# Optimization experiments

Measured on AMD Instinct MI355X. Metric: run time of the kernel, lower is better.

Reference implementation:

```python
import jax, jax.numpy as jnp
import numpy as np

B, S, D, H = 4, 2048, 1024, 16
HD = D // H  # 64

def setup_inputs() -> dict:
    key = jax.random.key(0)
    ks = jax.random.split(key, 6)
    scale = 1.0 / np.sqrt(D)
    return {
        "x": jax.random.normal(ks[0], (B, S, D), dtype=jnp.float32),
        "Wq": jax.random.normal(ks[1], (D, D), dtype=jnp.float32) * scale,
        "Wk": jax.random.normal(ks[2], (D, D), dtype=jnp.float32) * scale,
        "Wv": jax.random.normal(ks[3], (D, D), dtype=jnp.float32) * scale,
        "Wo": jax.random.normal(ks[4], (D, D), dtype=jnp.float32) * scale,
        "bo": jnp.zeros((D,), dtype=jnp.float32),
    }

def reference(x, Wq, Wk, Wv, Wo, bo):
    b, s, d = x.shape
    # projections (no bias for q/k/v, matching QKV_BIAS=False)
    q = (x @ Wq).reshape(b, s, H, HD).transpose(0, 2, 1, 3)  # [b,h,s,hd]
    k = (x @ Wk).reshape(b, s, H, HD).transpose(0, 2, 1, 3)
    v = (x @ Wv).reshape(b, s, H, HD).transpose(0, 2, 1, 3)
    scores = jnp.einsum('bhqd,bhkd->bhqk', q, k)  # [b,h,s,s]
    causal = jnp.tril(jnp.ones((s, s), dtype=bool))  # True where allowed
    scores = jnp.where(causal, scores, -jnp.inf)
    attn = jax.nn.softmax(scores / np.sqrt(HD), axis=-1)
    ctx = jnp.einsum('bhqk,bhkd->bhqd', attn, v)  # [b,h,s,hd]
    ctx = ctx.transpose(0, 2, 1, 3).reshape(b, s, d)
    return ctx @ Wo + bo
```

## Files before the change

kernel.cpp:

```cpp
#include <hip/hip_runtime.h>

#define BSZ 4
#define SEQ 2048
#define DIM 1024
#define NH  16
#define HD  64
#define QT  128
#define KT  64
#define PAD 72
#define NKT (DIM / 64)

typedef float v4f __attribute__((ext_vector_type(4)));
typedef short s8v __attribute__((ext_vector_type(8)));
typedef unsigned short u16;
typedef unsigned short u16x8 __attribute__((ext_vector_type(8)));
typedef unsigned short u16x4 __attribute__((ext_vector_type(4)));
typedef unsigned int u32;

__device__ __forceinline__ u16 f2bf(float f) {
  u32 u = __builtin_bit_cast(u32, f);
  u32 r = u + 0x7fffu + ((u >> 16) & 1u);
  return (u16)(r >> 16);
}
__device__ __forceinline__ float bf2f(u16 h) {
  return __builtin_bit_cast(float, (u32)h << 16);
}
__device__ __forceinline__ float fast_exp2(float x) {
#if __has_builtin(__builtin_amdgcn_exp2f)
  return __builtin_amdgcn_exp2f(x);
#else
  return exp2f(x);
#endif
}
__device__ __forceinline__ void gll16(const u16* g, u16* l) {
  __builtin_amdgcn_global_load_lds((const __attribute__((address_space(1))) void*)g,
                                   (__attribute__((address_space(3))) void*)l, 16, 0, 0);
}
__device__ __forceinline__ void wg_barrier() { asm volatile("s_barrier" ::: "memory"); }
#define WAITCNT_VM4   0xF74
#define WAITCNT_VM0   0xF70
#define WAITCNT_LGKM0 0xC07F

__global__ __launch_bounds__(256) void cast_bf16_kernel(const float* __restrict__ x,
                                                        u16* __restrict__ o, int n4) {
  int i = blockIdx.x * 256 + threadIdx.x;
  if (i >= n4) return;
  v4f v = reinterpret_cast<const v4f*>(x)[i];
  u16x4 r;
  #pragma unroll
  for (int c = 0; c < 4; c++) r[c] = f2bf(v[c]);
  reinterpret_cast<u16x4*>(o)[i] = r;
}

__global__ __launch_bounds__(256) void transpose_cast_kernel(const float* __restrict__ W0,
                                                             const float* __restrict__ W1,
                                                             const float* __restrict__ W2,
                                                             const float* __restrict__ W3,
                                                             u16* __restrict__ out) {
  const float* W = blockIdx.z == 0 ? W0 : blockIdx.z == 1 ? W1 : blockIdx.z == 2 ? W2 : W3;
  const float scale = (blockIdx.z == 0) ? 0.18033688011112042f : 1.0f;
  u16* T = out + (size_t)blockIdx.z * DIM * DIM;
  __shared__ float tile[32][33];
  int tx = threadIdx.x & 31, ty = threadIdx.x >> 5;
  int bn = blockIdx.x * 32, bk = blockIdx.y * 32;
  #pragma unroll
  for (int r = 0; r < 4; r++) {
    int k = bk + ty + r * 8;
    tile[ty + r * 8][tx] = W[(size_t)k * DIM + bn + tx];
  }
  __syncthreads();
  #pragma unroll
  for (int r = 0; r < 4; r++) {
    int n = bn + ty + r * 8;
    T[(size_t)n * DIM + bk + tx] = f2bf(tile[tx][ty + r * 8] * scale);
  }
}


#define ST_A(t_, kc_)                                                             \
  gll16(Ag0 + (t_) * 64 + (kc_) * 32, Aw0 + ((t_)&1) * 16384 + (kc_) * 8192);     \
  gll16(Ag1 + (t_) * 64 + (kc_) * 32, Aw1 + ((t_)&1) * 16384 + (kc_) * 8192);
#define ST_B(t_, kc_)                                                             \
  gll16(Bg0 + (t_) * 64 + (kc_) * 32, Bw0 + ((t_)&1) * 16384 + (kc_) * 8192);     \
  gll16(Bg1 + (t_) * 64 + (kc_) * 32, Bw1 + ((t_)&1) * 16384 + (kc_) * 8192);

#define PH(t_, kc_, mh_, STAGES, TAILW)                                           \
  { const u16* Ab = AL + ((t_)&1) * 16384 + (kc_) * 8192 + aRd;                   \
    const u16* Bb = BL + ((t_)&1) * 16384 + (kc_) * 8192 + bRd;                   \
    s8v af[4], bf[4];                                                             \
    _Pragma("unroll") for (int i_ = 0; i_ < 4; i_++)                              \
      af[i_] = *(const s8v*)(Ab + ((mh_) * 4 + i_) * 512);                        \
    _Pragma("unroll") for (int j_ = 0; j_ < 4; j_++)                              \
      bf[j_] = *(const s8v*)(Bb + j_ * 512);                                      \
    STAGES                                                                        \
    wg_barrier();                                                                 \
    __builtin_amdgcn_s_waitcnt(WAITCNT_LGKM0);                                    \
    __builtin_amdgcn_s_setprio(1);                                                \
    _Pragma("unroll") for (int i_ = 0; i_ < 4; i_++)                              \
      _Pragma("unroll") for (int j_ = 0; j_ < 4; j_++)                            \
        acc[(mh_) * 4 + i_][j_] = __builtin_amdgcn_mfma_f32_16x16x32_bf16(        \
            af[i_], bf[j_], acc[(mh_) * 4 + i_][j_], 0, 0, 0);                    \
    __builtin_amdgcn_s_setprio(0);                                                \
    TAILW                                                                         \
    wg_barrier(); }

#define GEMM256_CORE()                                                            \
  extern __shared__ __align__(16) u16 lds[];                                      \
  const int t = threadIdx.x;                                                      \
  const int lane = t & 63, w = t >> 6;                                            \
  const int waveM = w >> 2, waveN = w & 3;                                        \
  const int quad = lane >> 4, l16 = lane & 15;                                    \
  const int sR = lane & 15, sC = lane >> 4;                                       \
  u16* AL = lds;                                                                  \
  u16* BL = lds + 32768;                                                          \
  v4f acc[8][4];                                                                  \
  _Pragma("unroll") for (int i = 0; i < 8; i++)                                   \
    _Pragma("unroll") for (int j = 0; j < 4; j++)                                 \
      acc[i][j] = (v4f){0.f, 0.f, 0.f, 0.f};                                      \
  const u16* Ag0 = A + (size_t)(m0 + w * 32 + sR) * DIM + sC * 8;                 \
  const u16* Ag1 = A + (size_t)(m0 + w * 32 + 16 + sR) * DIM + sC * 8;            \
  const u16* Bg0 = Bt + (size_t)(n0 + w * 32 + sR) * DIM + sC * 8;                \
  const u16* Bg1 = Bt + (size_t)(n0 + w * 32 + 16 + sR) * DIM + sC * 8;           \
  u16* Aw0 = AL + (w * 2 + 0) * 512;                                              \
  u16* Aw1 = AL + (w * 2 + 1) * 512;                                              \
  u16* Bw0 = BL + (w * 2 + 0) * 512;                                              \
  u16* Bw1 = BL + (w * 2 + 1) * 512;                                              \
  const int aRd = waveM * 4096 + quad * 128 + l16 * 8;                            \
  const int bRd = waveN * 2048 + quad * 128 + l16 * 8;                            \
  ST_A(0, 0) ST_B(0, 0) ST_A(0, 1) ST_B(0, 1) ST_A(1, 0) ST_B(1, 0)              \
  __builtin_amdgcn_s_waitcnt(WAITCNT_VM4);                                        \
  wg_barrier();                                                                   \
  _Pragma("unroll 2") for (int kt = 0; kt < NKT - 2; kt++) {                      \
    PH(kt, 0, 0, ST_A(kt + 1, 1), )                                               \
    PH(kt, 0, 1, ST_B(kt + 1, 1), )                                               \
    PH(kt, 1, 0, ST_A(kt + 2, 0), )                                               \
    PH(kt, 1, 1, ST_B(kt + 2, 0), __builtin_amdgcn_s_waitcnt(WAITCNT_VM4);)       \
  }                                                                               \
  PH(NKT - 2, 0, 0, ST_A(NKT - 1, 1), )                                           \
  PH(NKT - 2, 0, 1, ST_B(NKT - 1, 1), )                                           \
  PH(NKT - 2, 1, 0, , )                                                           \
  PH(NKT - 2, 1, 1, , __builtin_amdgcn_s_waitcnt(WAITCNT_VM0);)                   \
  PH(NKT - 1, 0, 0, , )                                                           \
  PH(NKT - 1, 0, 1, , )                                                           \
  PH(NKT - 1, 1, 0, , )                                                           \
  PH(NKT - 1, 1, 1, , )

__global__ __launch_bounds__(512, 2) void gemm_qkv(const u16* __restrict__ A, const u16* __restrict__ Wt,
                                                   u16* __restrict__ Qb, u16* __restrict__ Kb,
                                                   u16* __restrict__ Vtg) {
  const int bid = blockIdx.x;
  const int swz = (bid & 7) * 48 + (bid >> 3);
  const int z = swz >> 7;
  const int rem = swz & 127;
  const int m0 = (rem >> 2) * 256;
  const int n0 = (rem & 3) * 256;
  const u16* Bt = Wt + (size_t)z * DIM * DIM;
  GEMM256_CORE()
  if (z == 2) {
    #pragma unroll
    for (int mi = 0; mi < 8; mi++) {
      #pragma unroll
      for (int ni = 0; ni < 4; ni++) {
        int gm0 = m0 + waveM * 128 + mi * 16 + quad * 4;
        int gn = n0 + waveN * 64 + ni * 16 + l16;
        int b = gm0 >> 11, s0 = gm0 & (SEQ - 1), hh = gn >> 6, d = gn & (HD - 1);
        u16x4 o;
        #pragma unroll
        for (int r = 0; r < 4; r++) o[r] = f2bf(acc[mi][ni][r]);
        *(u16x4*)(Vtg + ((size_t)(b * NH + hh) * HD + d) * SEQ + s0) = o;
      }
    }
  } else {
    u16* C = (z == 0) ? Qb : Kb;
    #pragma unroll
    for (int mi = 0; mi < 8; mi++) {
      #pragma unroll
      for (int ni = 0; ni < 4; ni++) {
        int gn = n0 + waveN * 64 + ni * 16 + l16;
        #pragma unroll
        for (int r = 0; r < 4; r++) {
          int gm = m0 + waveM * 128 + mi * 16 + quad * 4 + r;
          C[(size_t)gm * DIM + gn] = f2bf(acc[mi][ni][r]);
        }
      }
    }
  }
}

__global__ __launch_bounds__(512, 2) void gemm_proj(const u16* __restrict__ A, const u16* __restrict__ Bt,
                                                    float* __restrict__ Cf, const float* __restrict__ bias) {
  const int bid = blockIdx.x;
  const int swz = (bid & 7) * 16 + (bid >> 3);
  const int m0 = (swz >> 2) * 256;
  const int n0 = (swz & 3) * 256;
  GEMM256_CORE()
  #pragma unroll
  for (int ni = 0; ni < 4; ni++) {
    int gn = n0 + waveN * 64 + ni * 16 + l16;
    float bv = bias[gn];
    #pragma unroll
    for (int mi = 0; mi < 8; mi++) {
      #pragma unroll
      for (int r = 0; r < 4; r++) {
        int gm = m0 + waveM * 128 + mi * 16 + quad * 4 + r;
        Cf[(size_t)gm * DIM + gn] = acc[mi][ni][r] + bv;
      }
    }
  }
}

__global__ __launch_bounds__(256, 3) void flash_attn_mfma(const u16* __restrict__ Qb,
                                                          const u16* __restrict__ Kb,
                                                          const u16* __restrict__ Vtg,
                                                          u16* __restrict__ Ob) {
  const int h = blockIdx.x, px = blockIdx.y, bb = blockIdx.z;
  const int t = threadIdx.x;
  const int lane = t & 63, w = t >> 6;
  const int quad = lane >> 4, l16 = lane & 15;

  __shared__ u16 QPs[QT * PAD];
  __shared__ u16 Ks[KT * PAD];
  __shared__ u16 Vs[HD * PAD];

  const size_t qkbase = (size_t)bb * SEQ * DIM + h * HD;
  const size_t vbase = ((size_t)bb * NH + h) * (size_t)HD * SEQ;

  const int vrow = t >> 2, scol = (t & 3) * 16;
  const int krow = ((vrow >> 5) + 2 * ((vrow >> 2) & 1)) * 16 + ((vrow >> 3) & 3) * 4 + (vrow & 3);

  for (int pass = 0; pass < 2; pass++) {
    const int qi = (pass == 0) ? px : (SEQ / QT - 1 - px);
    const int q0 = qi * QT;
    const int wq = q0 + w * 32;
    const int ntiles = 2 * qi + 2;

    __syncthreads();

    {
      const int r = t >> 1, c0 = (t & 1) * 32;
      const u16* src = Qb + qkbase + (size_t)(q0 + r) * DIM + c0;
      #pragma unroll
      for (int ch = 0; ch < 4; ch++)
        *(u16x8*)(QPs + r * PAD + c0 + ch * 8) = *(const u16x8*)(src + ch * 8);
    }
    __syncthreads();

    s8v qf[2][2];
    #pragma unroll
    for (int ni = 0; ni < 2; ni++)
      #pragma unroll
      for (int kc = 0; kc < 2; kc++)
        qf[ni][kc] = *(const s8v*)(QPs + (w * 32 + ni * 16 + l16) * PAD + kc * 32 + quad * 8);

    u16x8 kr0, kr1, vr0, vr1;
    {
      const u16* kp = Kb + qkbase + (size_t)vrow * DIM + scol;
      kr0 = *(const u16x8*)kp; kr1 = *(const u16x8*)(kp + 8);
      const u16* vp = Vtg + vbase + (size_t)vrow * SEQ + scol;
      vr0 = *(const u16x8*)vp; vr1 = *(const u16x8*)(vp + 8);
    }

    float mrun[2] = {-1e30f, -1e30f}, lrun[2] = {0.f, 0.f};
    v4f O[4][2];
    #pragma unroll
    for (int di = 0; di < 4; di++)
      #pragma unroll
      for (int ni = 0; ni < 2; ni++) O[di][ni] = (v4f){0.f, 0.f, 0.f, 0.f};

    for (int it = 0; it < ntiles; ++it) {
      const int kv0 = it * KT;
      __syncthreads();
      *(u16x8*)(Ks + krow * PAD + scol) = kr0;
      *(u16x8*)(Ks + krow * PAD + scol + 8) = kr1;
      *(u16x8*)(Vs + vrow * PAD + scol) = vr0;
      *(u16x8*)(Vs + vrow * PAD + scol + 8) = vr1;
      __syncthreads();
      if (it + 1 < ntiles) {
        const int nkv = kv0 + KT;
        const u16* kp = Kb + qkbase + (size_t)(nkv + vrow) * DIM + scol;
        kr0 = *(const u16x8*)kp; kr1 = *(const u16x8*)(kp + 8);
        const u16* vp = Vtg + vbase + (size_t)vrow * SEQ + nkv + scol;
        vr0 = *(const u16x8*)vp; vr1 = *(const u16x8*)(vp + 8);
      }
      if (kv0 > wq + 31) continue;

      v4f sc[4][2];
      #pragma unroll
      for (int mi = 0; mi < 4; mi++)
        #pragma unroll
        for (int ni = 0; ni < 2; ni++) sc[mi][ni] = (v4f){0.f, 0.f, 0.f, 0.f};
      #pragma unroll
      for (int kc = 0; kc < 2; kc++) {
        #pragma unroll
        for (int mi = 0; mi < 4; mi++) {
          s8v kf = *(const s8v*)(Ks + (mi * 16 + l16) * PAD + kc * 32 + quad * 8);
          sc[mi][0] = __builtin_amdgcn_mfma_f32_16x16x32_bf16(kf, qf[0][kc], sc[mi][0], 0, 0, 0);
          sc[mi][1] = __builtin_amdgcn_mfma_f32_16x16x32_bf16(kf, qf[1][kc], sc[mi][1], 0, 0, 0);
        }
      }

      if (kv0 + KT > wq) {
        #pragma unroll
        for (int mi = 0; mi < 4; mi++) {
          const int kvb = kv0 + (mi & 1) * 32 + quad * 8 + (mi >> 1) * 4;
          #pragma unroll
          for (int ni = 0; ni < 2; ni++) {
            const int qg = wq + ni * 16 + l16;
            #pragma unroll
            for (int r = 0; r < 4; r++)
              if (kvb + r > qg) sc[mi][ni][r] = -1e30f;
          }
        }
      }

      float alpha[2];
      #pragma unroll
      for (int ni = 0; ni < 2; ni++) {
        float mx = -1e30f;
        #pragma unroll
        for (int mi = 0; mi < 4; mi++)
          #pragma unroll
          for (int r = 0; r < 4; r++) mx = fmaxf(mx, sc[mi][ni][r]);
        mx = fmaxf(mx, __shfl_xor(mx, 16, 64));
        mx = fmaxf(mx, __shfl_xor(mx, 32, 64));
        const float mnew = fmaxf(mrun[ni], mx);
        alpha[ni] = fast_exp2(mrun[ni] - mnew);
        mrun[ni] = mnew;
        float rsum = 0.f;
        #pragma unroll
        for (int mi = 0; mi < 4; mi++)
          #pragma unroll
          for (int r = 0; r < 4; r++) {
            float p = fast_exp2(sc[mi][ni][r] - mnew);
            sc[mi][ni][r] = p;
            rsum += p;
          }
        rsum += __shfl_xor(rsum, 16, 64);
        rsum += __shfl_xor(rsum, 32, 64);
        lrun[ni] = lrun[ni] * alpha[ni] + rsum;
      }
      #pragma unroll
      for (int di = 0; di < 4; di++)
        #pragma unroll
        for (int ni = 0; ni < 2; ni++)
          #pragma unroll
          for (int r = 0; r < 4; r++) O[di][ni][r] *= alpha[ni];

      s8v pf[2][2];
      #pragma unroll
      for (int ni = 0; ni < 2; ni++)
        #pragma unroll
        for (int kc = 0; kc < 2; kc++)
          #pragma unroll
          for (int j = 0; j < 8; j++)
            pf[ni][kc][j] = (short)f2bf(sc[kc + 2 * (j >> 2)][ni][j & 3]);

      #pragma unroll
      for (int kc = 0; kc < 2; kc++) {
        #pragma unroll
        for (int di = 0; di < 4; di++) {
          s8v vf = *(const s8v*)(Vs + (di * 16 + l16) * PAD + kc * 32 + quad * 8);
          O[di][0] = __builtin_amdgcn_mfma_f32_16x16x32_bf16(vf, pf[0][kc], O[di][0], 0, 0, 0);
          O[di][1] = __builtin_amdgcn_mfma_f32_16x16x32_bf16(vf, pf[1][kc], O[di][1], 0, 0, 0);
        }
      }
    }

    const float inv0 = 1.f / lrun[0], inv1 = 1.f / lrun[1];
    #pragma unroll
    for (int di = 0; di < 4; di++)
      #pragma unroll
      for (int ni = 0; ni < 2; ni++) {
        const float inv = ni ? inv1 : inv0;
        #pragma unroll
        for (int r = 0; r < 4; r++)
          QPs[(w * 32 + ni * 16 + l16) * PAD + di * 16 + quad * 4 + r] = f2bf(O[di][ni][r] * inv);
      }
    __syncthreads();
    {
      const int r = t >> 1, c0 = (t & 1) * 32;
      u16* dst = Ob + qkbase + (size_t)(q0 + r) * DIM + c0;
      #pragma unroll
      for (int ch = 0; ch < 4; ch++)
        *(u16x8*)(dst + ch * 8) = *(const u16x8*)(QPs + r * PAD + c0 + ch * 8);
    }
  }
}

extern "C" void kernel_launch(void* const* d_in, const int* in_sizes, int n_in,
                              void* d_out, int out_size, void* d_ws, size_t ws_size,
                              hipStream_t stream) {
  (void)in_sizes; (void)n_in; (void)out_size; (void)ws_size;
  const float* x  = (const float*)d_in[0];
  const float* Wq = (const float*)d_in[1];
  const float* Wk = (const float*)d_in[2];
  const float* Wv = (const float*)d_in[3];
  const float* Wo = (const float*)d_in[4];
  const float* bo = (const float*)d_in[5];
  float* out = (float*)d_out;

  static bool lds_attr_done = false;
  if (!lds_attr_done) {
    hipFuncSetAttribute(reinterpret_cast<const void*>(gemm_qkv),
                        hipFuncAttributeMaxDynamicSharedMemorySize, 131072);
    hipFuncSetAttribute(reinterpret_cast<const void*>(gemm_proj),
                        hipFuncAttributeMaxDynamicSharedMemorySize, 131072);
    lds_attr_done = true;
  }

  char* ws = (char*)d_ws;
  const size_t MB = 1024ull * 1024ull;
  u16* Xb  = (u16*)(ws);
  u16* Wt  = (u16*)(ws + 16 * MB);
  u16* Qb  = (u16*)(ws + 24 * MB);
  u16* Kb  = (u16*)(ws + 40 * MB);
  u16* Vtg = (u16*)(ws + 56 * MB);
  u16* Cb  = (u16*)(ws + 72 * MB);

  const int NTOK = BSZ * SEQ;
  const int n4 = NTOK * DIM / 4;
  cast_bf16_kernel<<<(n4 + 255) / 256, 256, 0, stream>>>(x, Xb, n4);
  transpose_cast_kernel<<<dim3(32, 32, 4), 256, 0, stream>>>(Wq, Wk, Wv, Wo, Wt);

  gemm_qkv<<<dim3(384), 512, 131072, stream>>>(Xb, Wt, Qb, Kb, Vtg);

  flash_attn_mfma<<<dim3(NH, SEQ / QT / 2, BSZ), 256, 0, stream>>>(Qb, Kb, Vtg, Cb);

  gemm_proj<<<dim3(128), 512, 131072, stream>>>(Cb, Wt + 3ull * DIM * DIM, out, bo);
}
```

Baseline: 284.4 us.

## Retile GEMMs to 256x128 with 3-stage pipeline, lazy softmax rescale, packed bf16 cvt

The QKV and output-projection GEMMs move from 256x256 tiles with a double buffer to 256x128 tiles with a triple-buffered LDS pipeline. This doubles the number of workgroups, which improves CU fill for the small projection GEMM, and changes the wait counts. The flash-attention softmax now skips rescaling O and l when the new row max exceeds the running max by no more than 8 (log2 units), which saves multiplies but risks larger intermediate values. Float-to-bf16 conversion now uses the hardware v_cvt_pk_bf16_f32 instruction instead of integer rounding code. LDS use rises to 144KB per block, and it is unclear whether two blocks still fit per CU.

Result: faster. 266.2 us (-6.4%).

```diff
diff --git a/kernel.cpp b/kernel.cpp
--- a/kernel.cpp
+++ b/kernel.cpp
@@ -16,15 +16,18 @@
 typedef unsigned short u16x8 __attribute__((ext_vector_type(8)));
 typedef unsigned short u16x4 __attribute__((ext_vector_type(4)));
 typedef unsigned int u32;
+typedef unsigned int u32x2 __attribute__((ext_vector_type(2)));
+typedef unsigned int u32x4 __attribute__((ext_vector_type(4)));
 
 __device__ __forceinline__ u16 f2bf(float f) {
   u32 u = __builtin_bit_cast(u32, f);
   u32 r = u + 0x7fffu + ((u >> 16) & 1u);
   return (u16)(r >> 16);
 }
-__device__ __forceinline__ float bf2f(u16 h) {
-  return __builtin_bit_cast(float, (u32)h << 16);
-}
+__device__ __forceinline__ u32 cvtpk(float lo, float hi) {
+  u32 r; asm("v_cvt_pk_bf16_f32 %0, %1, %2" : "=v"(r) : "v"(lo), "v"(hi)); return r;
+}
+__device__ __forceinline__ u16 f2bf1(float f) { return (u16)cvtpk(f, f); }
 __device__ __forceinline__ float fast_exp2(float x) {
 #if __has_builtin(__builtin_amdgcn_exp2f)
   return __builtin_amdgcn_exp2f(x);
@@ -37,9 +40,9 @@
                                    (__attribute__((address_space(3))) void*)l, 16, 0, 0);
 }
 __device__ __forceinline__ void wg_barrier() { asm volatile("s_barrier" ::: "memory"); }
-#define WAITCNT_VM4   0xF74
-#define WAITCNT_VM0   0xF70
 #define WAITCNT_LGKM0 0xC07F
+#define VMW6 __builtin_amdgcn_s_waitcnt(0xF76);
+#define VMW0 __builtin_amdgcn_s_waitcnt(0xF70);
 
 __global__ __launch_bounds__(256) void cast_bf16_kernel(const float* __restrict__ x,
                                                         u16* __restrict__ o, int n4) {
@@ -77,110 +80,108 @@
 }
 
 
-#define ST_A(t_, kc_)                                                             \
-  gll16(Ag0 + (t_) * 64 + (kc_) * 32, Aw0 + ((t_)&1) * 16384 + (kc_) * 8192);     \
-  gll16(Ag1 + (t_) * 64 + (kc_) * 32, Aw1 + ((t_)&1) * 16384 + (kc_) * 8192);
-#define ST_B(t_, kc_)                                                             \
-  gll16(Bg0 + (t_) * 64 + (kc_) * 32, Bw0 + ((t_)&1) * 16384 + (kc_) * 8192);     \
-  gll16(Bg1 + (t_) * 64 + (kc_) * 32, Bw1 + ((t_)&1) * 16384 + (kc_) * 8192);
-
-#define PH(t_, kc_, mh_, STAGES, TAILW)                                           \
-  { const u16* Ab = AL + ((t_)&1) * 16384 + (kc_) * 8192 + aRd;                   \
-    const u16* Bb = BL + ((t_)&1) * 16384 + (kc_) * 8192 + bRd;                   \
-    s8v af[4], bf[4];                                                             \
-    _Pragma("unroll") for (int i_ = 0; i_ < 4; i_++)                              \
-      af[i_] = *(const s8v*)(Ab + ((mh_) * 4 + i_) * 512);                        \
-    _Pragma("unroll") for (int j_ = 0; j_ < 4; j_++)                              \
-      bf[j_] = *(const s8v*)(Bb + j_ * 512);                                      \
+#define ST_TILE(t_, s_)                                                           \
+  gll16(Ag0 + (t_) * 64,      AW0 + (s_) * 16384);                                \
+  gll16(Ag1 + (t_) * 64,      AW1 + (s_) * 16384);                                \
+  gll16(Ag0 + (t_) * 64 + 32, AW0 + (s_) * 16384 + 8192);                         \
+  gll16(Ag1 + (t_) * 64 + 32, AW1 + (s_) * 16384 + 8192);                         \
+  gll16(Bg0 + (t_) * 64,      BW0 + (s_) * 8192);                                 \
+  gll16(Bg0 + (t_) * 64 + 32, BW0 + (s_) * 8192 + 4096);
+
+#define PH(t_, s_, STAGES, VMW)                                                   \
+  { const u16* Ab = AL + (s_) * 16384 + aRd;                                      \
+    const u16* Bb = BL + (s_) * 8192 + bRd;                                       \
+    s8v af[2][4], bf[2][4];                                                       \
+    _Pragma("unroll") for (int kc_ = 0; kc_ < 2; kc_++) {                         \
+      _Pragma("unroll") for (int i_ = 0; i_ < 4; i_++)                            \
+        af[kc_][i_] = *(const s8v*)(Ab + kc_ * 8192 + i_ * 512);                  \
+      _Pragma("unroll") for (int j_ = 0; j_ < 4; j_++)                            \
+        bf[kc_][j_] = *(const s8v*)(Bb + kc_ * 4096 + j_ * 512);                  \
+    }                                                                             \
     STAGES                                                                        \
+    VMW                                                                           \
     wg_barrier();                                                                 \
     __builtin_amdgcn_s_waitcnt(WAITCNT_LGKM0);                                    \
     __builtin_amdgcn_s_setprio(1);                                                \
-    _Pragma("unroll") for (int i_ = 0; i_ < 4; i_++)                              \
-      _Pragma("unroll") for (int j_ = 0; j_ < 4; j_++)                            \
-        acc[(mh_) * 4 + i_][j_] = __builtin_amdgcn_mfma_f32_16x16x32_bf16(        \
-            af[i_], bf[j_], acc[(mh_) * 4 + i_][j_], 0, 0, 0);                    \
+    _Pragma("unroll") for (int kc_ = 0; kc_ < 2; kc_++)                           \
+      _Pragma("unroll") for (int i_ = 0; i_ < 4; i_++)                            \
+        _Pragma("unroll") for (int j_ = 0; j_ < 4; j_++)                          \
+          acc[i_][j_] = __builtin_amdgcn_mfma_f32_16x16x32_bf16(                  \
+              af[kc_][i_], bf[kc_][j_], acc[i_][j_], 0, 0, 0);                    \
     __builtin_amdgcn_s_setprio(0);                                                \
-    TAILW                                                                         \
     wg_barrier(); }
 
-#define GEMM256_CORE()                                                            \
+#define GEMM256x128_CORE()                                                        \
   extern __shared__ __align__(16) u16 lds[];                                      \
   const int t = threadIdx.x;                                                      \
   const int lane = t & 63, w = t >> 6;                                            \
-  const int waveM = w >> 2, waveN = w & 3;                                        \
+  const int waveM = w >> 1, waveN = w & 1;                                        \
   const int quad = lane >> 4, l16 = lane & 15;                                    \
   const int sR = lane & 15, sC = lane >> 4;                                       \
   u16* AL = lds;                                                                  \
-  u16* BL = lds + 32768;                                                          \
-  v4f acc[8][4];                                                                  \
-  _Pragma("unroll") for (int i = 0; i < 8; i++)                                   \
+  u16* BL = lds + 49152;                                                          \
+  v4f acc[4][4];                                                                  \
+  _Pragma("unroll") for (int i = 0; i < 4; i++)                                   \
     _Pragma("unroll") for (int j = 0; j < 4; j++)                                 \
       acc[i][j] = (v4f){0.f, 0.f, 0.f, 0.f};                                      \
   const u16* Ag0 = A + (size_t)(m0 + w * 32 + sR) * DIM + sC * 8;                 \
-  const u16* Ag1 = A + (size_t)(m0 + w * 32 + 16 + sR) * DIM + sC * 8;            \
-  const u16* Bg0 = Bt + (size_t)(n0 + w * 32 + sR) * DIM + sC * 8;                \
-  const u16* Bg1 = Bt + (size_t)(n0 + w * 32 + 16 + sR) * DIM + sC * 8;           \
-  u16* Aw0 = AL + (w * 2 + 0) * 512;                                              \
-  u16* Aw1 = AL + (w * 2 + 1) * 512;                                              \
-  u16* Bw0 = BL + (w * 2 + 0) * 512;                                              \
-  u16* Bw1 = BL + (w * 2 + 1) * 512;                                              \
-  const int aRd = waveM * 4096 + quad * 128 + l16 * 8;                            \
+  const u16* Ag1 = Ag0 + 16 * DIM;                                                \
+  const u16* Bg0 = Bt + (size_t)(n0 + w * 16 + sR) * DIM + sC * 8;                \
+  u16* AW0 = AL + w * 1024;                                                       \
+  u16* AW1 = AL + w * 1024 + 512;                                                 \
+  u16* BW0 = BL + w * 512;                                                        \
+  const int aRd = waveM * 2048 + quad * 128 + l16 * 8;                            \
   const int bRd = waveN * 2048 + quad * 128 + l16 * 8;                            \
-  ST_A(0, 0) ST_B(0, 0) ST_A(0, 1) ST_B(0, 1) ST_A(1, 0) ST_B(1, 0)              \
-  __builtin_amdgcn_s_waitcnt(WAITCNT_VM4);                                        \
+  ST_TILE(0, 0) ST_TILE(1, 1)                                                     \
+  VMW6                                                                            \
   wg_barrier();                                                                   \
-  _Pragma("unroll 2") for (int kt = 0; kt < NKT - 2; kt++) {                      \
-    PH(kt, 0, 0, ST_A(kt + 1, 1), )                                               \
-    PH(kt, 0, 1, ST_B(kt + 1, 1), )                                               \
-    PH(kt, 1, 0, ST_A(kt + 2, 0), )                                               \
-    PH(kt, 1, 1, ST_B(kt + 2, 0), __builtin_amdgcn_s_waitcnt(WAITCNT_VM4);)       \
+  _Pragma("unroll") for (int t3 = 0; t3 < 12; t3 += 3) {                          \
+    PH(t3 + 0, 0, ST_TILE(t3 + 2, 2), VMW6)                                       \
+    PH(t3 + 1, 1, ST_TILE(t3 + 3, 0), VMW6)                                       \
+    PH(t3 + 2, 2, ST_TILE(t3 + 4, 1), VMW6)                                       \
   }                                                                               \
-  PH(NKT - 2, 0, 0, ST_A(NKT - 1, 1), )                                           \
-  PH(NKT - 2, 0, 1, ST_B(NKT - 1, 1), )                                           \
-  PH(NKT - 2, 1, 0, , )                                                           \
-  PH(NKT - 2, 1, 1, , __builtin_amdgcn_s_waitcnt(WAITCNT_VM0);)                   \
-  PH(NKT - 1, 0, 0, , )                                                           \
-  PH(NKT - 1, 0, 1, , )                                                           \
-  PH(NKT - 1, 1, 0, , )                                                           \
-  PH(NKT - 1, 1, 1, , )
+  PH(12, 0, ST_TILE(14, 2), VMW6)                                                 \
+  PH(13, 1, ST_TILE(15, 0), VMW6)                                                 \
+  PH(14, 2, , VMW0)                                                               \
+  PH(15, 0, , )
 
 __global__ __launch_bounds__(512, 2) void gemm_qkv(const u16* __restrict__ A, const u16* __restrict__ Wt,
                                                    u16* __restrict__ Qb, u16* __restrict__ Kb,
                                                    u16* __restrict__ Vtg) {
   const int bid = blockIdx.x;
-  const int swz = (bid & 7) * 48 + (bid >> 3);
-  const int z = swz >> 7;
-  const int rem = swz & 127;
-  const int m0 = (rem >> 2) * 256;
-  const int n0 = (rem & 3) * 256;
+  const int swz = (bid & 7) * 96 + (bid >> 3);
+  const int z = swz >> 8;
+  const int rem = swz & 255;
+  const int m0 = (rem >> 3) * 256;
+  const int n0 = (rem & 7) * 128;
   const u16* Bt = Wt + (size_t)z * DIM * DIM;
-  GEMM256_CORE()
+  GEMM256x128_CORE()
   if (z == 2) {
     #pragma unroll
-    for (int mi = 0; mi < 8; mi++) {
+    for (int mi = 0; mi < 4; mi++) {
       #pragma unroll
       for (int ni = 0; ni < 4; ni++) {
-        int gm0 = m0 + waveM * 128 + mi * 16 + quad * 4;
+        int gm0 = m0 + waveM * 64 + mi * 16 + quad * 4;
         int gn = n0 + waveN * 64 + ni * 16 + l16;
         int b = gm0 >> 11, s0 = gm0 & (SEQ - 1), hh = gn >> 6, d = gn & (HD - 1);
-        u16x4 o;
-        #pragma unroll
-        for (int r = 0; r < 4; r++) o[r] = f2bf(acc[mi][ni][r]);
-        *(u16x4*)(Vtg + ((size_t)(b * NH + hh) * HD + d) * SEQ + s0) = o;
+        u32x2 pw;
+        pw[0] = cvtpk(acc[mi][ni][0], acc[mi][ni][1]);
+        pw[1] = cvtpk(acc[mi][ni][2], acc[mi][ni][3]);
+        *(u16x4*)(Vtg + ((size_t)(b * NH + hh) * HD + d) * SEQ + s0) =
+            __builtin_bit_cast(u16x4, pw);
       }
     }
   } else {
     u16* C = (z == 0) ? Qb : Kb;
     #pragma unroll
-    for (int mi = 0; mi < 8; mi++) {
+    for (int mi = 0; mi < 4; mi++) {
       #pragma unroll
       for (int ni = 0; ni < 4; ni++) {
         int gn = n0 + waveN * 64 + ni * 16 + l16;
         #pragma unroll
         for (int r = 0; r < 4; r++) {
-          int gm = m0 + waveM * 128 + mi * 16 + quad * 4 + r;
-          C[(size_t)gm * DIM + gn] = f2bf(acc[mi][ni][r]);
+          int gm = m0 + waveM * 64 + mi * 16 + quad * 4 + r;
+          C[(size_t)gm * DIM + gn] = f2bf1(acc[mi][ni][r]);
         }
       }
     }
@@ -190,19 +191,19 @@
 __global__ __launch_bounds__(512, 2) void gemm_proj(const u16* __restrict__ A, const u16* __restrict__ Bt,
                                                     float* __restrict__ Cf, const float* __restrict__ bias) {
   const int bid = blockIdx.x;
-  const int swz = (bid & 7) * 16 + (bid >> 3);
-  const int m0 = (swz >> 2) * 256;
-  const int n0 = (swz & 3) * 256;
-  GEMM256_CORE()
+  const int swz = (bid & 7) * 32 + (bid >> 3);
+  const int m0 = (swz >> 3) * 256;
+  const int n0 = (swz & 7) * 128;
+  GEMM256x128_CORE()
   #pragma unroll
   for (int ni = 0; ni < 4; ni++) {
     int gn = n0 + waveN * 64 + ni * 16 + l16;
     float bv = bias[gn];
     #pragma unroll
-    for (int mi = 0; mi < 8; mi++) {
+    for (int mi = 0; mi < 4; mi++) {
       #pragma unroll
       for (int r = 0; r < 4; r++) {
-        int gm = m0 + waveM * 128 + mi * 16 + quad * 4 + r;
+        int gm = m0 + waveM * 64 + mi * 16 + quad * 4 + r;
         Cf[(size_t)gm * DIM + gn] = acc[mi][ni][r] + bv;
       }
     }
@@ -313,47 +314,63 @@
         }
       }
 
-      float alpha[2];
+      float mx[2];
       #pragma unroll
       for (int ni = 0; ni < 2; ni++) {
-        float mx = -1e30f;
+        float m = -1e30f;
         #pragma unroll
         for (int mi = 0; mi < 4; mi++)
           #pragma unroll
-          for (int r = 0; r < 4; r++) mx = fmaxf(mx, sc[mi][ni][r]);
-        mx = fmaxf(mx, __shfl_xor(mx, 16, 64));
-        mx = fmaxf(mx, __shfl_xor(mx, 32, 64));
-        const float mnew = fmaxf(mrun[ni], mx);
-        alpha[ni] = fast_exp2(mrun[ni] - mnew);
-        mrun[ni] = mnew;
+          for (int r = 0; r < 4; r++) m = fmaxf(m, sc[mi][ni][r]);
+        m = fmaxf(m, __shfl_xor(m, 16, 64));
+        m = fmaxf(m, __shfl_xor(m, 32, 64));
+        mx[ni] = m;
+      }
+      const bool defer = __all((mx[0] <= mrun[0] + 8.f) && (mx[1] <= mrun[1] + 8.f));
+      if (!defer) {
+        float alpha[2];
+        #pragma unroll
+        for (int ni = 0; ni < 2; ni++) {
+          const float mnew = fmaxf(mrun[ni], mx[ni]);
+          alpha[ni] = fast_exp2(mrun[ni] - mnew);
+          mrun[ni] = mnew;
+          lrun[ni] *= alpha[ni];
+        }
+        #pragma unroll
+        for (int di = 0; di < 4; di++)
+          #pragma unroll
+          for (int ni = 0; ni < 2; ni++)
+            #pragma unroll
+            for (int r = 0; r < 4; r++) O[di][ni][r] *= alpha[ni];
+      }
+      #pragma unroll
+      for (int ni = 0; ni < 2; ni++) {
         float rsum = 0.f;
         #pragma unroll
         for (int mi = 0; mi < 4; mi++)
           #pragma unroll
           for (int r = 0; r < 4; r++) {
-            float p = fast_exp2(sc[mi][ni][r] - mnew);
+            float p = fast_exp2(sc[mi][ni][r] - mrun[ni]);
             sc[mi][ni][r] = p;
             rsum += p;
           }
         rsum += __shfl_xor(rsum, 16, 64);
         rsum += __shfl_xor(rsum, 32, 64);
-        lrun[ni] = lrun[ni] * alpha[ni] + rsum;
-      }
-      #pragma unroll
-      for (int di = 0; di < 4; di++)
-        #pragma unroll
-        for (int ni = 0; ni < 2; ni++)
-          #pragma unroll
-          for (int r = 0; r < 4; r++) O[di][ni][r] *= alpha[ni];
+        lrun[ni] += rsum;
+      }
 
       s8v pf[2][2];
       #pragma unroll
       for (int ni = 0; ni < 2; ni++)
         #pragma unroll
-        for (int kc = 0; kc < 2; kc++)
-          #pragma unroll
-          for (int j = 0; j < 8; j++)
-            pf[ni][kc][j] = (short)f2bf(sc[kc + 2 * (j >> 2)][ni][j & 3]);
+        for (int kc = 0; kc < 2; kc++) {
+          u32x4 wds;
+          wds[0] = cvtpk(sc[kc][ni][0], sc[kc][ni][1]);
+          wds[1] = cvtpk(sc[kc][ni][2], sc[kc][ni][3]);
+          wds[2] = cvtpk(sc[kc + 2][ni][0], sc[kc + 2][ni][1]);
+          wds[3] = cvtpk(sc[kc + 2][ni][2], sc[kc + 2][ni][3]);
+          pf[ni][kc] = __builtin_bit_cast(s8v, wds);
+        }
 
       #pragma unroll
       for (int kc = 0; kc < 2; kc++) {
@@ -374,7 +391,7 @@
         const float inv = ni ? inv1 : inv0;
         #pragma unroll
         for (int r = 0; r < 4; r++)
-          QPs[(w * 32 + ni * 16 + l16) * PAD + di * 16 + quad * 4 + r] = f2bf(O[di][ni][r] * inv);
+          QPs[(w * 32 + ni * 16 + l16) * PAD + di * 16 + quad * 4 + r] = f2bf1(O[di][ni][r] * inv);
       }
     __syncthreads();
     {
@@ -402,9 +419,9 @@
   static bool lds_attr_done = false;
   if (!lds_attr_done) {
     hipFuncSetAttribute(reinterpret_cast<const void*>(gemm_qkv),
-                        hipFuncAttributeMaxDynamicSharedMemorySize, 131072);
+                        hipFuncAttributeMaxDynamicSharedMemorySize, 147456);
     hipFuncSetAttribute(reinterpret_cast<const void*>(gemm_proj),
-                        hipFuncAttributeMaxDynamicSharedMemorySize, 131072);
+                        hipFuncAttributeMaxDynamicSharedMemorySize, 147456);
     lds_attr_done = true;
   }
 
@@ -422,9 +439,9 @@
   cast_bf16_kernel<<<(n4 + 255) / 256, 256, 0, stream>>>(x, Xb, n4);
   transpose_cast_kernel<<<dim3(32, 32, 4), 256, 0, stream>>>(Wq, Wk, Wv, Wo, Wt);
 
-  gemm_qkv<<<dim3(384), 512, 131072, stream>>>(Xb, Wt, Qb, Kb, Vtg);
+  gemm_qkv<<<dim3(768), 512, 147456, stream>>>(Xb, Wt, Qb, Kb, Vtg);
 
   flash_attn_mfma<<<dim3(NH, SEQ / QT / 2, BSZ), 256, 0, stream>>>(Qb, Kb, Vtg, Cb);
 
-  gemm_proj<<<dim3(128), 512, 131072, stream>>>(Cb, Wt + 3ull * DIM * DIM, out, bo);
-}
+  gemm_proj<<<dim3(256), 512, 147456, stream>>>(Cb, Wt + 3ull * DIM * DIM, out, bo);
+}
```
